# Optimization experiments

Measured on AMD Instinct MI355X. Metric: run time of the kernel, lower is better.

Reference implementation:

```python
import jax, jax.numpy as jnp
import numpy as np

N_NODES = 100000
N_EDGES = 1600000
NODES_PER_GRAPH = 100  # equal-sized graphs -> batch = arange // 100
POOL_K = 30


def setup_inputs() -> dict:
    key = jax.random.key(0)
    ks = jax.random.split(key, 8)
    F_IN, H1, H2, OUT = 128, 128, 128, 64
    x = jax.random.normal(ks[0], (N_NODES, F_IN), dtype=jnp.float32)
    edge_index = jax.random.randint(ks[1], (2, N_EDGES), 0, N_NODES, dtype=jnp.int64)
    batch = (jnp.arange(N_NODES, dtype=jnp.int64) // NODES_PER_GRAPH)
    # Glorot-ish init for weights, zero bias (as PyG GCNConv defaults)
    W1 = jax.random.normal(ks[2], (F_IN, H1), dtype=jnp.float32) / np.sqrt(F_IN)
    b1 = jnp.zeros((H1,), dtype=jnp.float32)
    W2 = jax.random.normal(ks[3], (H1, H2), dtype=jnp.float32) / np.sqrt(H1)
    b2 = jnp.zeros((H2,), dtype=jnp.float32)
    W3 = jax.random.normal(ks[4], (H2, OUT), dtype=jnp.float32) / np.sqrt(H2)
    b3 = jnp.zeros((OUT,), dtype=jnp.float32)
    return {"x": x, "edge_index": edge_index, "batch": batch,
            "W1": W1, "b1": b1, "W2": W2, "b2": b2, "W3": W3, "b3": b3}


def _gcn_conv(x, src, dst, W, b):
    """PyG GCNConv: xW, add self-loops, symmetric D^-1/2 A D^-1/2 scatter-add, +bias."""
    n = x.shape[0]
    loops = jnp.arange(n, dtype=src.dtype)
    row = jnp.concatenate([src, loops])  # message source
    col = jnp.concatenate([dst, loops])  # aggregation target
    xw = x @ W
    deg = jax.ops.segment_sum(jnp.ones(col.shape[0], x.dtype), col, num_segments=n)
    dinv = jnp.where(deg > 0, jax.lax.rsqrt(deg), 0.0)
    norm = dinv[row] * dinv[col]  # [E+N]
    out = jax.ops.segment_sum(xw[row] * norm[:, None], col, num_segments=n)
    return out + b


def _sort_pool(x, k):
    """global_sort_pool: per-graph descending sort by last channel, take top-k, flatten.
    Graphs are equal-sized and contiguous, so reshape to [B, P, C]."""
    n, c = x.shape
    xb = x.reshape(n // NODES_PER_GRAPH, NODES_PER_GRAPH, c)  # [B, P, C]
    order = jnp.argsort(-xb[..., -1], axis=1)[:, :k]          # [B, k]
    topk = jnp.take_along_axis(xb, order[..., None], axis=1)  # [B, k, C]
    return topk.reshape(topk.shape[0], k * c)


def reference(x, edge_index, batch, W1, b1, W2, b2, W3, b3):
    src, dst = edge_index[0], edge_index[1]
    h = jax.nn.relu(_gcn_conv(x, src, dst, W1, b1))
    h = jax.nn.relu(_gcn_conv(h, src, dst, W2, b2))
    h = _gcn_conv(h, src, dst, W3, b3)
    return _sort_pool(h, POOL_K)
```

## Files before the change

### kernel.cpp

```cpp
#include <hip/hip_runtime.h>
#include <math.h>

static inline size_t ws_align(size_t x) { return (x + 255) & ~(size_t)255; }

__global__ void count_kernel(const int* __restrict__ dst, int* __restrict__ counts, int E) {
  int e = blockIdx.x * 256 + threadIdx.x;
  if (e < E) atomicAdd(&counts[dst[e]], 1);
}

__global__ __launch_bounds__(256) void scanA_kernel(const int* __restrict__ counts,
    int* __restrict__ bsums, int n) {
  __shared__ int red[4];
  const int base = blockIdx.x * 1024;
  const int tid = threadIdx.x;
  int s = 0;
  #pragma unroll
  for (int u = 0; u < 4; ++u) {
    int i = base + u * 256 + tid;
    s += (i < n) ? counts[i] : 0;
  }
  #pragma unroll
  for (int m = 1; m < 64; m <<= 1) s += __shfl_xor(s, m, 64);
  if ((tid & 63) == 0) red[tid >> 6] = s;
  __syncthreads();
  if (tid == 0) bsums[blockIdx.x] = red[0] + red[1] + red[2] + red[3];
}

__global__ __launch_bounds__(128) void scanB_kernel(int* __restrict__ bsums, int nb) {
  __shared__ int tmp[129];
  int tid = threadIdx.x;
  tmp[tid] = (tid < nb) ? bsums[tid] : 0;
  __syncthreads();
  if (tid == 0) {
    int run = 0;
    for (int i = 0; i < nb; ++i) { int v = tmp[i]; tmp[i] = run; run += v; }
  }
  __syncthreads();
  if (tid < nb) bsums[tid] = tmp[tid];
}

__global__ __launch_bounds__(1024) void scanC_kernel(const int* __restrict__ counts,
    const int* __restrict__ bsums, int* __restrict__ offsets, int* __restrict__ cursor,
    double* __restrict__ dinv, int n) {
  __shared__ int warpsums[16];
  const int tid = threadIdx.x;
  const int lane = tid & 63, wid = tid >> 6;
  const int i = blockIdx.x * 1024 + tid;
  int v = (i < n) ? counts[i] : 0;
  int x = v;
  #pragma unroll
  for (int d = 1; d < 64; d <<= 1) {
    int y = __shfl_up(x, d, 64);
    if (lane >= d) x += y;
  }
  if (lane == 63) warpsums[wid] = x;
  __syncthreads();
  if (wid == 0) {
    int w = (lane < 16) ? warpsums[lane] : 0;
    #pragma unroll
    for (int d = 1; d < 16; d <<= 1) {
      int y = __shfl_up(w, d, 64);
      if (lane >= d) w += y;
    }
    if (lane < 16) warpsums[lane] = w;
  }
  __syncthreads();
  int excl = bsums[blockIdx.x] + x - v + (wid > 0 ? warpsums[wid - 1] : 0);
  if (i < n) {
    offsets[i] = excl;
    cursor[i] = excl;
    dinv[i] = 1.0 / sqrt((double)(v + 1));
    if (i == n - 1) offsets[n] = excl + v;
  }
}

__global__ void scatter_kernel(const int* __restrict__ src, const int* __restrict__ dst,
    int* __restrict__ cursor, int* __restrict__ srcs, float* __restrict__ ew,
    const double* __restrict__ dinv, int E, int use_ew) {
  int e = blockIdx.x * 256 + threadIdx.x;
  if (e < E) {
    int s = src[e], d = dst[e];
    int p = atomicAdd(&cursor[d], 1);
    srcs[p] = s;
    if (use_ew) ew[p] = (float)(dinv[s] * dinv[d]);
  }
}

__global__ void cvtW_kernel(const float* __restrict__ W1, const float* __restrict__ W2,
    const float* __restrict__ W3, double* __restrict__ W1d, double* __restrict__ W2d,
    double* __restrict__ W3d) {
  int i = blockIdx.x * 256 + threadIdx.x;
  if (i < 16384) { W1d[i] = (double)W1[i]; W2d[i] = (double)W2[i]; }
  if (i < 8192)  { W3d[i] = (double)W3[i]; }
}

template<int H, int MINW>
__global__ __launch_bounds__(256, MINW) void gemm_kernel(const float* __restrict__ X,
    const double* __restrict__ Wd, float* __restrict__ out, int N) {
  __shared__ float xs[128 * 64];
  const int tid  = threadIdx.x;
  const int row0 = blockIdx.x * 64;
  #pragma unroll
  for (int p = 0; p < 8; ++p) {
    int idx = p * 256 + tid;
    int r  = idx >> 5;
    int c4 = idx & 31;
    int grow = row0 + r;
    float4 v = make_float4(0.f, 0.f, 0.f, 0.f);
    if (grow < N) v = *(const float4*)(X + (size_t)grow * 128 + c4 * 4);
    const int g = r >> 2, s = r & 3;
    float vals[4] = {v.x, v.y, v.z, v.w};
    #pragma unroll
    for (int j = 0; j < 4; ++j) {
      int k = c4 * 4 + j;
      xs[k * 64 + ((g ^ (k & 15)) << 2) + s] = vals[j];
    }
  }
  __syncthreads();
  constexpr int CPT = H / 16;
  const int rowg = tid & 15;
  const int colg = tid >> 4;
  const float4* xsv = (const float4*)xs;
  const double* wbase = Wd + colg * CPT;

  double acc[4][CPT];
  #pragma unroll
  for (int j = 0; j < 4; ++j)
    #pragma unroll
    for (int h = 0; h < CPT; ++h) acc[j][h] = 0.0;

  float4 aA = xsv[(0 << 4) + (rowg ^ 0)];
  float4 aB;
  double bA[CPT], bB[CPT];
  #pragma unroll
  for (int q = 0; q < CPT / 2; ++q) {
    double2 t = *(const double2*)(wbase + 0 * H + q * 2);
    bA[2*q] = t.x; bA[2*q+1] = t.y;
  }

  #pragma unroll 1
  for (int k = 0; k < 128; k += 2) {
    aB = xsv[((k + 1) << 4) + (rowg ^ ((k + 1) & 15))];
    #pragma unroll
    for (int q = 0; q < CPT / 2; ++q) {
      double2 t = *(const double2*)(wbase + (size_t)(k + 1) * H + q * 2);
      bB[2*q] = t.x; bB[2*q+1] = t.y;
    }
    {
      double a0 = (double)aA.x, a1 = (double)aA.y, a2 = (double)aA.z, a3 = (double)aA.w;
      #pragma unroll
      for (int h = 0; h < CPT; ++h) {
        acc[0][h] = fma(a0, bA[h], acc[0][h]);
        acc[1][h] = fma(a1, bA[h], acc[1][h]);
        acc[2][h] = fma(a2, bA[h], acc[2][h]);
        acc[3][h] = fma(a3, bA[h], acc[3][h]);
      }
    }
    if (k + 2 < 128) {
      aA = xsv[((k + 2) << 4) + (rowg ^ ((k + 2) & 15))];
      #pragma unroll
      for (int q = 0; q < CPT / 2; ++q) {
        double2 t = *(const double2*)(wbase + (size_t)(k + 2) * H + q * 2);
        bA[2*q] = t.x; bA[2*q+1] = t.y;
      }
    }
    {
      double a0 = (double)aB.x, a1 = (double)aB.y, a2 = (double)aB.z, a3 = (double)aB.w;
      #pragma unroll
      for (int h = 0; h < CPT; ++h) {
        acc[0][h] = fma(a0, bB[h], acc[0][h]);
        acc[1][h] = fma(a1, bB[h], acc[1][h]);
        acc[2][h] = fma(a2, bB[h], acc[2][h]);
        acc[3][h] = fma(a3, bB[h], acc[3][h]);
      }
    }
  }
  #pragma unroll
  for (int j = 0; j < 4; ++j) {
    int grow = row0 + rowg * 4 + j;
    if (grow < N) {
      float* o = out + (size_t)grow * H + colg * CPT;
      #pragma unroll
      for (int q = 0; q < CPT / 4; ++q) {
        float4 v = make_float4((float)acc[j][q*4+0], (float)acc[j][q*4+1],
                               (float)acc[j][q*4+2], (float)acc[j][q*4+3]);
        *(float4*)(o + q * 4) = v;
      }
    }
  }
}

template<int C, bool RELU, bool USE_EW>
__global__ __launch_bounds__(256) void gather_kernel(const float* __restrict__ xw,
    const double* __restrict__ dinv, const int* __restrict__ offs,
    const int* __restrict__ srcs, const float* __restrict__ ew,
    const float* __restrict__ bias, float* __restrict__ out, int N) {
  constexpr int LPR = C / 4;
  constexpr int EPI = 64 / LPR;
  constexpr int U = 8;
  const int node = blockIdx.x * 4 + (threadIdx.x >> 6);
  if (node >= N) return;
  const int lane = threadIdx.x & 63;
  const int grp  = lane / LPR;
  const int c0   = (lane % LPR) * 4;
  const int e0 = offs[node], e1 = offs[node + 1];
  const double di = dinv[node];
  double a0 = 0.0, a1 = 0.0, a2 = 0.0, a3 = 0.0;

  for (int base = e0; base < e1; base += U * EPI) {
    int ss[U];
    double ww[U];
    float4 vv[U];
    #pragma unroll
    for (int u = 0; u < U; ++u) {
      int ee = base + u * EPI + grp;
      int cl = ee < e1 ? ee : e1 - 1;
      ss[u] = srcs[cl];
      if (USE_EW) ww[u] = (double)ew[cl];
    }
    #pragma unroll
    for (int u = 0; u < U; ++u) {
      vv[u] = *(const float4*)(xw + (size_t)ss[u] * C + c0);
      if (!USE_EW) ww[u] = dinv[ss[u]];
    }
    #pragma unroll
    for (int u = 0; u < U; ++u) {
      int ee = base + u * EPI + grp;
      double w = (ee < e1) ? ww[u] : 0.0;
      a0 = fma(w, (double)vv[u].x, a0);
      a1 = fma(w, (double)vv[u].y, a1);
      a2 = fma(w, (double)vv[u].z, a2);
      a3 = fma(w, (double)vv[u].w, a3);
    }
  }
  #pragma unroll
  for (int m = LPR; m < 64; m <<= 1) {
    a0 += __shfl_xor(a0, m, 64);
    a1 += __shfl_xor(a1, m, 64);
    a2 += __shfl_xor(a2, m, 64);
    a3 += __shfl_xor(a3, m, 64);
  }
  if (grp == 0) {
    const double d2 = di * di;
    float4 sv = *(const float4*)(xw + (size_t)node * C + c0);
    float4 bv = *(const float4*)(bias + c0);
    double o0, o1, o2, o3;
    if (USE_EW) {
      o0 = a0 + fma(d2, (double)sv.x, (double)bv.x);
      o1 = a1 + fma(d2, (double)sv.y, (double)bv.y);
      o2 = a2 + fma(d2, (double)sv.z, (double)bv.z);
      o3 = a3 + fma(d2, (double)sv.w, (double)bv.w);
    } else {
      o0 = fma(di, a0, fma(d2, (double)sv.x, (double)bv.x));
      o1 = fma(di, a1, fma(d2, (double)sv.y, (double)bv.y));
      o2 = fma(di, a2, fma(d2, (double)sv.z, (double)bv.z));
      o3 = fma(di, a3, fma(d2, (double)sv.w, (double)bv.w));
    }
    if (RELU) {
      o0 = o0 > 0.0 ? o0 : 0.0; o1 = o1 > 0.0 ? o1 : 0.0;
      o2 = o2 > 0.0 ? o2 : 0.0; o3 = o3 > 0.0 ? o3 : 0.0;
    }
    *(float4*)(out + (size_t)node * C + c0) =
        make_float4((float)o0, (float)o1, (float)o2, (float)o3);
  }
}

__global__ __launch_bounds__(128) void sortpool_kernel(const float* __restrict__ h,
    float* __restrict__ out) {
  __shared__ float sv[128];
  __shared__ int si[128];
  int g = blockIdx.x;
  int tid = threadIdx.x;
  const float* hg = h + (size_t)g * 100 * 64;
  if (tid < 100) {
    sv[tid] = hg[tid * 64 + 63];
    si[tid] = tid;
  } else {
    sv[tid] = -3.0e38f;
    si[tid] = 1 << 30;
  }
  __syncthreads();
  for (int k = 2; k <= 128; k <<= 1) {
    for (int j = k >> 1; j > 0; j >>= 1) {
      int i = tid;
      int l = i ^ j;
      if (l > i) {
        float va = sv[i], vb = sv[l];
        int ia = si[i], ib = si[l];
        bool a_before_b = (va > vb) || (va == vb && ia < ib);
        bool up = ((i & k) == 0);
        bool sw = up ? !a_before_b : a_before_b;
        if (sw) { sv[i] = vb; sv[l] = va; si[i] = ib; si[l] = ia; }
      }
      __syncthreads();
    }
  }
  for (int t = tid; t < 30 * 64; t += 128) {
    int kk = t >> 6;
    int c = t & 63;
    out[(size_t)g * (30 * 64) + t] = hg[si[kk] * 64 + c];
  }
}

extern "C" void kernel_launch(void* const* d_in, const int* in_sizes, int n_in,
                              void* d_out, int out_size, void* d_ws, size_t ws_size,
                              hipStream_t stream) {
  const float* x  = (const float*)d_in[0];
  const int*   ei = (const int*)d_in[1];
  const float* W1 = (const float*)d_in[3];
  const float* b1 = (const float*)d_in[4];
  const float* W2 = (const float*)d_in[5];
  const float* b2 = (const float*)d_in[6];
  const float* W3 = (const float*)d_in[7];
  const float* b3 = (const float*)d_in[8];

  const int N = in_sizes[0] / 128;
  const int E = in_sizes[1] / 2;
  const int* src = ei;
  const int* dst = ei + E;
  (void)n_in; (void)out_size;

  const int nb = (N + 1023) / 1024;

  char* ws = (char*)d_ws;
  size_t off = 0;
  auto alloc = [&](size_t bytes) { char* p = ws + off; off = ws_align(off + bytes); return p; };
  float*  xw      = (float*) alloc((size_t)N * 128 * 4);
  float*  h       = (float*) alloc((size_t)N * 128 * 4);
  double* dinv    = (double*)alloc((size_t)N * 8);
  int*    offsets = (int*)   alloc(((size_t)N + 1) * 4);
  int*    cursor  = (int*)   alloc((size_t)N * 4);
  int*    counts  = (int*)   alloc((size_t)N * 4);
  int*    srcs    = (int*)   alloc((size_t)E * 4);
  double* W1d     = (double*)alloc(16384 * 8);
  double* W2d     = (double*)alloc(16384 * 8);
  double* W3d     = (double*)alloc(8192 * 8);
  int*    bsums   = (int*)   alloc((size_t)(nb + 1) * 4);
  float*  ew      = (float*) alloc((size_t)E * 4);
  const bool use_ew = (off <= ws_size);

  hipMemsetAsync(counts, 0, (size_t)N * 4, stream);
  count_kernel<<<(E + 255) / 256, 256, 0, stream>>>(dst, counts, E);
  scanA_kernel<<<nb, 256, 0, stream>>>(counts, bsums, N);
  scanB_kernel<<<1, 128, 0, stream>>>(bsums, nb);
  scanC_kernel<<<nb, 1024, 0, stream>>>(counts, bsums, offsets, cursor, dinv, N);
  scatter_kernel<<<(E + 255) / 256, 256, 0, stream>>>(src, dst, cursor, srcs, ew, dinv, E, use_ew ? 1 : 0);
  cvtW_kernel<<<64, 256, 0, stream>>>(W1, W2, W3, W1d, W2d, W3d);

  const int gblocks  = (N + 63) / 64;
  const int nblocks4 = (N + 3) / 4;

  gemm_kernel<128, 3><<<gblocks, 256, 0, stream>>>(x, W1d, xw, N);
  if (use_ew) {
    gather_kernel<128, true,  true><<<nblocks4, 256, 0, stream>>>(xw, dinv, offsets, srcs, ew, b1, h, N);
    gemm_kernel<128, 3><<<gblocks, 256, 0, stream>>>(h, W2d, xw, N);
    gather_kernel<128, true,  true><<<nblocks4, 256, 0, stream>>>(xw, dinv, offsets, srcs, ew, b2, h, N);
    gemm_kernel<64, 4><<<gblocks, 256, 0, stream>>>(h, W3d, xw, N);
    gather_kernel<64,  false, true><<<nblocks4, 256, 0, stream>>>(xw, dinv, offsets, srcs, ew, b3, h, N);
  } else {
    gather_kernel<128, true,  false><<<nblocks4, 256, 0, stream>>>(xw, dinv, offsets, srcs, ew, b1, h, N);
    gemm_kernel<128, 3><<<gblocks, 256, 0, stream>>>(h, W2d, xw, N);
    gather_kernel<128, true,  false><<<nblocks4, 256, 0, stream>>>(xw, dinv, offsets, srcs, ew, b2, h, N);
    gemm_kernel<64, 4><<<gblocks, 256, 0, stream>>>(h, W3d, xw, N);
    gather_kernel<64,  false, false><<<nblocks4, 256, 0, stream>>>(xw, dinv, offsets, srcs, ew, b3, h, N);
  }
  sortpool_kernel<<<N / 100, 128, 0, stream>>>(h, (float*)d_out);
}
```

Before: 878.6 us.

## Use 512-thread GEMM blocks with fewer columns per thread and float weights

The GEMM now runs 512 threads per block, and each thread computes half as many output columns, which cuts the number of double-precision accumulator registers per thread. Weights are read directly as float and converted to double in registers, so the separate weight-conversion kernel and its double workspace copies are gone. The shared-memory tile switches from an XOR-swizzled layout to a padded (stride 68) layout. This is meant to raise occupancy and latency hiding for the FP64 FMA loop, in exchange for more weight loads per FMA and a conversion on every k step.

```diff
diff --git a/kernel.cpp b/kernel.cpp
--- a/kernel.cpp
+++ b/kernel.cpp
@@ -86,42 +86,30 @@
   }
 }
 
-__global__ void cvtW_kernel(const float* __restrict__ W1, const float* __restrict__ W2,
-    const float* __restrict__ W3, double* __restrict__ W1d, double* __restrict__ W2d,
-    double* __restrict__ W3d) {
-  int i = blockIdx.x * 256 + threadIdx.x;
-  if (i < 16384) { W1d[i] = (double)W1[i]; W2d[i] = (double)W2[i]; }
-  if (i < 8192)  { W3d[i] = (double)W3[i]; }
-}
-
-template<int H, int MINW>
-__global__ __launch_bounds__(256, MINW) void gemm_kernel(const float* __restrict__ X,
-    const double* __restrict__ Wd, float* __restrict__ out, int N) {
-  __shared__ float xs[128 * 64];
+template<int H>
+__global__ __launch_bounds__(512, 4) void gemm_kernel(const float* __restrict__ X,
+    const float* __restrict__ W, float* __restrict__ out, int N) {
+  __shared__ float xs[128 * 68];
   const int tid  = threadIdx.x;
   const int row0 = blockIdx.x * 64;
   #pragma unroll
-  for (int p = 0; p < 8; ++p) {
-    int idx = p * 256 + tid;
-    int r  = idx >> 5;
-    int c4 = idx & 31;
+  for (int p = 0; p < 4; ++p) {
+    int idx = p * 512 + tid;
+    int r  = idx & 63;
+    int c4 = idx >> 6;
     int grow = row0 + r;
     float4 v = make_float4(0.f, 0.f, 0.f, 0.f);
     if (grow < N) v = *(const float4*)(X + (size_t)grow * 128 + c4 * 4);
-    const int g = r >> 2, s = r & 3;
     float vals[4] = {v.x, v.y, v.z, v.w};
     #pragma unroll
-    for (int j = 0; j < 4; ++j) {
-      int k = c4 * 4 + j;
-      xs[k * 64 + ((g ^ (k & 15)) << 2) + s] = vals[j];
-    }
-  }
-  __syncthreads();
-  constexpr int CPT = H / 16;
+    for (int j = 0; j < 4; ++j)
+      xs[(4 * c4 + j) * 68 + r] = vals[j];
+  }
+  __syncthreads();
+  constexpr int CPT = H / 32;
   const int rowg = tid & 15;
   const int colg = tid >> 4;
-  const float4* xsv = (const float4*)xs;
-  const double* wbase = Wd + colg * CPT;
+  const float* wbase = W + colg * CPT;
 
   double acc[4][CPT];
   #pragma unroll
@@ -129,49 +117,46 @@
     #pragma unroll
     for (int h = 0; h < CPT; ++h) acc[j][h] = 0.0;
 
-  float4 aA = xsv[(0 << 4) + (rowg ^ 0)];
+  float4 aA = *(const float4*)(xs + 4 * rowg);
   float4 aB;
-  double bA[CPT], bB[CPT];
-  #pragma unroll
-  for (int q = 0; q < CPT / 2; ++q) {
-    double2 t = *(const double2*)(wbase + 0 * H + q * 2);
-    bA[2*q] = t.x; bA[2*q+1] = t.y;
-  }
+  float bA[CPT], bB[CPT];
+  #pragma unroll
+  for (int h = 0; h < CPT; ++h) bA[h] = wbase[h];
 
   #pragma unroll 1
   for (int k = 0; k < 128; k += 2) {
-    aB = xsv[((k + 1) << 4) + (rowg ^ ((k + 1) & 15))];
-    #pragma unroll
-    for (int q = 0; q < CPT / 2; ++q) {
-      double2 t = *(const double2*)(wbase + (size_t)(k + 1) * H + q * 2);
-      bB[2*q] = t.x; bB[2*q+1] = t.y;
-    }
+    aB = *(const float4*)(xs + (k + 1) * 68 + 4 * rowg);
+    #pragma unroll
+    for (int h = 0; h < CPT; ++h) bB[h] = wbase[(size_t)(k + 1) * H + h];
     {
       double a0 = (double)aA.x, a1 = (double)aA.y, a2 = (double)aA.z, a3 = (double)aA.w;
+      double b[CPT];
+      #pragma unroll
+      for (int h = 0; h < CPT; ++h) b[h] = (double)bA[h];
       #pragma unroll
       for (int h = 0; h < CPT; ++h) {
-        acc[0][h] = fma(a0, bA[h], acc[0][h]);
-        acc[1][h] = fma(a1, bA[h], acc[1][h]);
-        acc[2][h] = fma(a2, bA[h], acc[2][h]);
-        acc[3][h] = fma(a3, bA[h], acc[3][h]);
+        acc[0][h] = fma(a0, b[h], acc[0][h]);
+        acc[1][h] = fma(a1, b[h], acc[1][h]);
+        acc[2][h] = fma(a2, b[h], acc[2][h]);
+        acc[3][h] = fma(a3, b[h], acc[3][h]);
       }
     }
     if (k + 2 < 128) {
-      aA = xsv[((k + 2) << 4) + (rowg ^ ((k + 2) & 15))];
-      #pragma unroll
-      for (int q = 0; q < CPT / 2; ++q) {
-        double2 t = *(const double2*)(wbase + (size_t)(k + 2) * H + q * 2);
-        bA[2*q] = t.x; bA[2*q+1] = t.y;
-      }
+      aA = *(const float4*)(xs + (k + 2) * 68 + 4 * rowg);
+      #pragma unroll
+      for (int h = 0; h < CPT; ++h) bA[h] = wbase[(size_t)(k + 2) * H + h];
     }
     {
       double a0 = (double)aB.x, a1 = (double)aB.y, a2 = (double)aB.z, a3 = (double)aB.w;
+      double b[CPT];
+      #pragma unroll
+      for (int h = 0; h < CPT; ++h) b[h] = (double)bB[h];
       #pragma unroll
       for (int h = 0; h < CPT; ++h) {
-        acc[0][h] = fma(a0, bB[h], acc[0][h]);
-        acc[1][h] = fma(a1, bB[h], acc[1][h]);
-        acc[2][h] = fma(a2, bB[h], acc[2][h]);
-        acc[3][h] = fma(a3, bB[h], acc[3][h]);
+        acc[0][h] = fma(a0, b[h], acc[0][h]);
+        acc[1][h] = fma(a1, b[h], acc[1][h]);
+        acc[2][h] = fma(a2, b[h], acc[2][h]);
+        acc[3][h] = fma(a3, b[h], acc[3][h]);
       }
     }
   }
@@ -180,11 +165,13 @@
     int grow = row0 + rowg * 4 + j;
     if (grow < N) {
       float* o = out + (size_t)grow * H + colg * CPT;
-      #pragma unroll
-      for (int q = 0; q < CPT / 4; ++q) {
-        float4 v = make_float4((float)acc[j][q*4+0], (float)acc[j][q*4+1],
-                               (float)acc[j][q*4+2], (float)acc[j][q*4+3]);
-        *(float4*)(o + q * 4) = v;
+      if constexpr (CPT == 4) {
+        float4 v = make_float4((float)acc[j][0], (float)acc[j][1],
+                               (float)acc[j][2], (float)acc[j][3]);
+        *(float4*)o = v;
+      } else {
+        float2 v = make_float2((float)acc[j][0], (float)acc[j][1]);
+        *(float2*)o = v;
       }
     }
   }
@@ -332,9 +319,6 @@
   int*    cursor  = (int*)   alloc((size_t)N * 4);
   int*    counts  = (int*)   alloc((size_t)N * 4);
   int*    srcs    = (int*)   alloc((size_t)E * 4);
-  double* W1d     = (double*)alloc(16384 * 8);
-  double* W2d     = (double*)alloc(16384 * 8);
-  double* W3d     = (double*)alloc(8192 * 8);
   int*    bsums   = (int*)   alloc((size_t)(nb + 1) * 4);
   float*  ew      = (float*) alloc((size_t)E * 4);
   const bool use_ew = (off <= ws_size);
@@ -345,23 +329,22 @@
   scanB_kernel<<<1, 128, 0, stream>>>(bsums, nb);
   scanC_kernel<<<nb, 1024, 0, stream>>>(counts, bsums, offsets, cursor, dinv, N);
   scatter_kernel<<<(E + 255) / 256, 256, 0, stream>>>(src, dst, cursor, srcs, ew, dinv, E, use_ew ? 1 : 0);
-  cvtW_kernel<<<64, 256, 0, stream>>>(W1, W2, W3, W1d, W2d, W3d);
 
   const int gblocks  = (N + 63) / 64;
   const int nblocks4 = (N + 3) / 4;
 
-  gemm_kernel<128, 3><<<gblocks, 256, 0, stream>>>(x, W1d, xw, N);
+  gemm_kernel<128><<<gblocks, 512, 0, stream>>>(x, W1, xw, N);
   if (use_ew) {
     gather_kernel<128, true,  true><<<nblocks4, 256, 0, stream>>>(xw, dinv, offsets, srcs, ew, b1, h, N);
-    gemm_kernel<128, 3><<<gblocks, 256, 0, stream>>>(h, W2d, xw, N);
+    gemm_kernel<128><<<gblocks, 512, 0, stream>>>(h, W2, xw, N);
     gather_kernel<128, true,  true><<<nblocks4, 256, 0, stream>>>(xw, dinv, offsets, srcs, ew, b2, h, N);
-    gemm_kernel<64, 4><<<gblocks, 256, 0, stream>>>(h, W3d, xw, N);
+    gemm_kernel<64 ><<<gblocks, 512, 0, stream>>>(h, W3, xw, N);
     gather_kernel<64,  false, true><<<nblocks4, 256, 0, stream>>>(xw, dinv, offsets, srcs, ew, b3, h, N);
   } else {
     gather_kernel<128, true,  false><<<nblocks4, 256, 0, stream>>>(xw, dinv, offsets, srcs, ew, b1, h, N);
-    gemm_kernel<128, 3><<<gblocks, 256, 0, stream>>>(h, W2d, xw, N);
+    gemm_kernel<128><<<gblocks, 512, 0, stream>>>(h, W2, xw, N);
     gather_kernel<128, true,  false><<<nblocks4, 256, 0, stream>>>(xw, dinv, offsets, srcs, ew, b2, h, N);
-    gemm_kernel<64, 4><<<gblocks, 256, 0, stream>>>(h, W3d, xw, N);
+    gemm_kernel<64 ><<<gblocks, 512, 0, stream>>>(h, W3, xw, N);
     gather_kernel<64,  false, false><<<nblocks4, 256, 0, stream>>>(xw, dinv, offsets, srcs, ew, b3, h, N);
   }
   sortpool_kernel<<<N / 100, 128, 0, stream>>>(h, (float*)d_out);
```

Result: no change. 883.0 us (+0.5%).
